# Performance work log

Measured on AMD Instinct MI355X. Metric: run time of the kernel, lower is better.

The kernel has to match this reference:

```python
import jax, jax.numpy as jnp
import numpy as np

TOKENS, IN_F, OUT_F = 8192, 4096, 4096

def setup_inputs() -> dict:
    key = jax.random.key(0)
    k1, k2, k3, k4 = jax.random.split(key, 4)
    x = jax.random.randint(k1, (TOKENS, IN_F), -128, 128, dtype=jnp.int32).astype(jnp.int8)
    weight = jax.random.randint(k2, (OUT_F, IN_F), -128, 128, dtype=jnp.int32).astype(jnp.int8)
    # per-output-channel static dequant scale (small positive values, as for int8 quant)
    dequant_scale = (jax.random.uniform(k3, (OUT_F,), dtype=jnp.float32) * 0.01 + 1e-4)
    bias = (jax.random.normal(k4, (OUT_F,), dtype=jnp.float32) * 0.02).astype(jnp.float16)
    return {"x": x, "weight": weight, "dequant_scale": dequant_scale, "bias": bias}

def reference(x, weight, dequant_scale, bias):
    acc = jnp.matmul(x.astype(jnp.int32), weight.T.astype(jnp.int32))
    # fused epilogue: per-channel dequant + bias add, cast to fp16 output
    out = (acc.astype(jnp.float32) * dequant_scale[None, :]
           + bias.astype(jnp.float32)[None, :]).astype(jnp.float16)
    # module's forward returns (output, bias)
    return (out, bias)
```

## Files before the change

kernel.cpp:

```cpp
#include <hip/hip_runtime.h>
#include <hip/hip_fp16.h>

#define TOKENS 8192
#define IN_F   4096
#define OUT_F  4096
#define NK64   (IN_F / 64)

#define REG    16384
#define BUFSZ  (2 * REG)
typedef __attribute__((ext_vector_type(4))) int i32x4;

__global__ void prep_kernel(const int* __restrict__ xs, const int* __restrict__ ws,
                            const float* __restrict__ bias,
                            int4* __restrict__ xp, int4* __restrict__ wp,
                            float* __restrict__ out_tail) {
    const int NA = (TOKENS / 256) * 64 * 1024;
    const int NB = (OUT_F  / 256) * 64 * 1024;
    const int gid = blockIdx.x * blockDim.x + threadIdx.x;
    const int stride = gridDim.x * blockDim.x;
    for (int s = gid; s < NA + NB; s += stride) {
        const int* src; int4* dst; int t2;
        if (s < NA) { src = xs; dst = xp; t2 = s; }
        else        { src = ws; dst = wp; t2 = s - NA; }
        const int slot = t2 & 1023;
        const int blk  = t2 >> 10;
        const int f    = slot >> 6;
        const int l    = slot & 63;
        const int row  = (blk >> 6) * 256 + f * 16 + (l & 15);
        const int k0   = (blk & 63) * 64 + ((l >> 4) << 4);
        const int* p   = src + (size_t)row * IN_F + k0;
        int4 a = *(const int4*)(p + 0);
        int4 b = *(const int4*)(p + 4);
        int4 c = *(const int4*)(p + 8);
        int4 e = *(const int4*)(p + 12);
        int4 o;
        o.x = (int)((a.x & 0xffu) | ((a.y & 0xffu) << 8) | ((a.z & 0xffu) << 16) | ((a.w & 0xffu) << 24));
        o.y = (int)((b.x & 0xffu) | ((b.y & 0xffu) << 8) | ((b.z & 0xffu) << 16) | ((b.w & 0xffu) << 24));
        o.z = (int)((c.x & 0xffu) | ((c.y & 0xffu) << 8) | ((c.z & 0xffu) << 16) | ((c.w & 0xffu) << 24));
        o.w = (int)((e.x & 0xffu) | ((e.y & 0xffu) << 8) | ((e.z & 0xffu) << 16) | ((e.w & 0xffu) << 24));
        dst[t2] = o;
    }
    if (gid < OUT_F) out_tail[gid] = bias[gid];
}

__global__ __launch_bounds__(512, 2) void gemm_i8_kernel(
    const char* __restrict__ A,
    const char* __restrict__ B,
    const float* __restrict__ scale,
    const float* __restrict__ bias,
    float* __restrict__ out)
{
    __shared__ char lds[4 * BUFSZ];

    const int tid  = threadIdx.x;
    const int wid  = tid >> 6;
    const int lane = tid & 63;
    const int wm   = wid >> 2;
    const int wn   = wid & 3;

    const int bid   = blockIdx.x;
    const int xcd   = bid & 7;
    const int j9    = bid >> 3;
    const int rect  = (j9 >> 5) * 8 + xcd;
    const int jj    = j9 & 31;
    const int tm    = (rect & 3) * 8 + (jj & 7);
    const int tn    = (rect >> 2) * 4 + (jj >> 3);

    const char* ag = A + (size_t)tm * (64 * 16384);
    const char* bg = B + (size_t)tn * (64 * 16384);
    const int   ldst = tid * 16;

#define STAGE(r, t)                                                                        \
    do {                                                                                   \
        _Pragma("unroll")                                                                  \
        for (int i = 0; i < 2; ++i) {                                                      \
            size_t go = (size_t)(t) * 16384 + i * 8192 + ldst;                             \
            __builtin_amdgcn_global_load_lds(                                              \
                (const __attribute__((address_space(1))) void*)(ag + go),                  \
                (__attribute__((address_space(3))) void*)(&lds[(r) * BUFSZ +               \
                                                              i * 8192 + ldst]),           \
                16, 0, 0);                                                                 \
            __builtin_amdgcn_global_load_lds(                                              \
                (const __attribute__((address_space(1))) void*)(bg + go),                  \
                (__attribute__((address_space(3))) void*)(&lds[(r) * BUFSZ + REG +         \
                                                              i * 8192 + ldst]),           \
                16, 0, 0);                                                                 \
        }                                                                                  \
    } while (0)

    const int aoff = wm * 8 * 1024 + lane * 16;
    const int boff = REG + wn * 4 * 1024 + lane * 16;

    i32x4 acc[8][4];
#pragma unroll
    for (int m = 0; m < 8; ++m)
#pragma unroll
        for (int n = 0; n < 4; ++n)
            acc[m][n] = (i32x4){0, 0, 0, 0};

    STAGE(0, 0);
    STAGE(1, 1);
    STAGE(2, 2);

#define TILE(t, VM, DOSTAGE)                                                               \
    do {                                                                                   \
        asm volatile("s_waitcnt vmcnt(" #VM ")" ::: "memory");                             \
        __builtin_amdgcn_s_barrier();                                                      \
        __builtin_amdgcn_sched_barrier(0);                                                 \
        const char* Lr = &lds[((t) & 3) * BUFSZ];                                          \
        i32x4 af[8], bf[4];                                                                \
        _Pragma("unroll")                                                                  \
        for (int n = 0; n < 4; ++n)                                                        \
            bf[n] = *(const i32x4*)(Lr + boff + n * 1024);                                 \
        _Pragma("unroll")                                                                  \
        for (int m = 0; m < 8; ++m)                                                        \
            af[m] = *(const i32x4*)(Lr + aoff + m * 1024);                                 \
        if (DOSTAGE) STAGE(((t) + 3) & 3, (t) + 3);                                        \
        __builtin_amdgcn_s_setprio(1);                                                     \
        _Pragma("unroll")                                                                  \
        for (int m = 0; m < 8; ++m)                                                        \
            _Pragma("unroll")                                                              \
            for (int n = 0; n < 4; ++n)                                                    \
                acc[m][n] = __builtin_amdgcn_mfma_i32_16x16x64_i8(                         \
                    af[m], bf[n], acc[m][n], 0, 0, 0);                                     \
        __builtin_amdgcn_s_setprio(0);                                                     \
    } while (0)

#pragma unroll 1
    for (int t = 0; t <= NK64 - 4; ++t) TILE(t, 8, 1);
    TILE(NK64 - 3, 8, 0);
    TILE(NK64 - 2, 4, 0);
    TILE(NK64 - 1, 0, 0);

    const int col  = tn * 256 + wn * 64 + (lane & 15);
    const int row0 = tm * 256 + wm * 128 + ((lane >> 4) << 2);
    float sc[4], bi[4];
#pragma unroll
    for (int n = 0; n < 4; ++n) {
        sc[n] = scale[col + n * 16];
        bi[n] = bias[col + n * 16];
    }
#pragma unroll
    for (int m = 0; m < 8; ++m)
#pragma unroll
        for (int n = 0; n < 4; ++n)
#pragma unroll
            for (int r = 0; r < 4; ++r) {
                float v = (float)acc[m][n][r] * sc[n] + bi[n];
                out[(size_t)(row0 + m * 16 + r) * OUT_F + col + n * 16] =
                    (float)__float2half_rn(v);
            }
#undef STAGE
#undef TILE
}

extern "C" void kernel_launch(void* const* d_in, const int* in_sizes, int n_in,
                              void* d_out, int out_size, void* d_ws, size_t ws_size,
                              hipStream_t stream) {
    const int*   x_i32 = (const int*)d_in[0];
    const int*   w_i32 = (const int*)d_in[1];
    const float* scale = (const float*)d_in[2];
    const float* bias  = (const float*)d_in[3];
    float*       out   = (float*)d_out;

    char* xp = (char*)d_ws;
    char* wp = xp + (size_t)TOKENS * IN_F;

    prep_kernel<<<3072, 256, 0, stream>>>(x_i32, w_i32, bias,
                                          (int4*)xp, (int4*)wp, out + (size_t)TOKENS * OUT_F);

    gemm_i8_kernel<<<(TOKENS / 256) * (OUT_F / 256), 512, 0, stream>>>(xp, wp, scale, bias, out);
}
```

Baseline: 183.9 us.

## Double-buffer LDS fragments in registers and interleave ds_reads with MFMAs

Each k-tile's A/B fragments are now prefetched from LDS into a second register set while the current tile's MFMAs run, instead of being loaded right before use. The main loop is unrolled by two to ping-pong the register buffers, and the vmcnt wait is tightened so tile t+1 is resident before it is prefetched. sched_group_barrier hints interleave the LDS reads and global-to-LDS loads with the MFMA stream to hide LDS latency. The cost is roughly double the fragment registers under a 512-thread, 2-block launch bound, which risks spills or lower occupancy.

```diff
diff --git a/kernel.cpp b/kernel.cpp
--- a/kernel.cpp
+++ b/kernel.cpp
@@ -98,39 +98,63 @@
         for (int n = 0; n < 4; ++n)
             acc[m][n] = (i32x4){0, 0, 0, 0};
 
-    STAGE(0, 0);
-    STAGE(1, 1);
-    STAGE(2, 2);
+    i32x4 afA[8], bfA[4], afB[8], bfB[4];
 
-#define TILE(t, VM, DOSTAGE)                                                               \
+#define PREFETCH(s, AF, BF)                                                                \
+    do {                                                                                   \
+        const char* Lp = &lds[((s) & 3) * BUFSZ];                                          \
+        _Pragma("unroll")                                                                  \
+        for (int n = 0; n < 4; ++n)                                                        \
+            BF[n] = *(const i32x4*)(Lp + boff + n * 1024);                                 \
+        _Pragma("unroll")                                                                  \
+        for (int m = 0; m < 8; ++m)                                                        \
+            AF[m] = *(const i32x4*)(Lp + aoff + m * 1024);                                 \
+    } while (0)
+
+#define TILE(t, VM, DOSTAGE, DOPREF, AF, BF, AFN, BFN)                                     \
     do {                                                                                   \
         asm volatile("s_waitcnt vmcnt(" #VM ")" ::: "memory");                             \
         __builtin_amdgcn_s_barrier();                                                      \
+        asm volatile("s_waitcnt lgkmcnt(0)" ::: "memory");                                 \
         __builtin_amdgcn_sched_barrier(0);                                                 \
-        const char* Lr = &lds[((t) & 3) * BUFSZ];                                          \
-        i32x4 af[8], bf[4];                                                                \
-        _Pragma("unroll")                                                                  \
-        for (int n = 0; n < 4; ++n)                                                        \
-            bf[n] = *(const i32x4*)(Lr + boff + n * 1024);                                 \
-        _Pragma("unroll")                                                                  \
-        for (int m = 0; m < 8; ++m)                                                        \
-            af[m] = *(const i32x4*)(Lr + aoff + m * 1024);                                 \
         if (DOSTAGE) STAGE(((t) + 3) & 3, (t) + 3);                                        \
+        if (DOPREF) PREFETCH((t) + 1, AFN, BFN);                                           \
         __builtin_amdgcn_s_setprio(1);                                                     \
         _Pragma("unroll")                                                                  \
         for (int m = 0; m < 8; ++m)                                                        \
             _Pragma("unroll")                                                              \
             for (int n = 0; n < 4; ++n)                                                    \
                 acc[m][n] = __builtin_amdgcn_mfma_i32_16x16x64_i8(                         \
-                    af[m], bf[n], acc[m][n], 0, 0, 0);                                     \
+                    AF[m], BF[n], acc[m][n], 0, 0, 0);                                     \
         __builtin_amdgcn_s_setprio(0);                                                     \
+        if (DOSTAGE) __builtin_amdgcn_sched_group_barrier(0x070, 4, 0);                    \
+        if (DOPREF) {                                                                      \
+            _Pragma("unroll")                                                              \
+            for (int g = 0; g < 12; ++g) {                                                 \
+                __builtin_amdgcn_sched_group_barrier(0x008, 2, 0);                         \
+                __builtin_amdgcn_sched_group_barrier(0x100, 1, 0);                         \
+            }                                                                              \
+            __builtin_amdgcn_sched_group_barrier(0x008, 8, 0);                             \
+        }                                                                                  \
     } while (0)
 
+    STAGE(0, 0);
+    STAGE(1, 1);
+    STAGE(2, 2);
+    asm volatile("s_waitcnt vmcnt(8)" ::: "memory");
+    __builtin_amdgcn_s_barrier();
+    __builtin_amdgcn_sched_barrier(0);
+    PREFETCH(0, afA, bfA);
+
 #pragma unroll 1
-    for (int t = 0; t <= NK64 - 4; ++t) TILE(t, 8, 1);
-    TILE(NK64 - 3, 8, 0);
-    TILE(NK64 - 2, 4, 0);
-    TILE(NK64 - 1, 0, 0);
+    for (int t2 = 0; t2 < NK64 - 4; t2 += 2) {
+        TILE(t2 + 0, 4, 1, 1, afA, bfA, afB, bfB);
+        TILE(t2 + 1, 4, 1, 1, afB, bfB, afA, bfA);
+    }
+    TILE(NK64 - 4, 4, 1, 1, afA, bfA, afB, bfB);
+    TILE(NK64 - 3, 4, 0, 1, afB, bfB, afA, bfA);
+    TILE(NK64 - 2, 0, 0, 1, afA, bfA, afB, bfB);
+    TILE(NK64 - 1, 0, 0, 0, afB, bfB, afA, bfA);
 
     const int col  = tn * 256 + wn * 64 + (lane & 15);
     const int row0 = tm * 256 + wm * 128 + ((lane >> 4) << 2);
@@ -151,6 +175,7 @@
                     (float)__float2half_rn(v);
             }
 #undef STAGE
+#undef PREFETCH
 #undef TILE
 }
 
```

New measurement: 187.0 us. Within noise of the previous version (+1.6%).
